# Performance work log

Hardware: AMD Instinct MI355X
Metric: run time of the kernel (lower is better)

## Reference

```python
import jax, jax.numpy as jnp
import numpy as np

B, L, D, H, W = 2, 4096, 1024, 16, 128
E = D // H

def _ln(x, g, b):
    m = jnp.mean(x, axis=-1, keepdims=True)
    v = jnp.mean((x - m) ** 2, axis=-1, keepdims=True)
    return (x - m) / jnp.sqrt(v + 1e-5) * g + b

def _swa(xn, Wqkv, bqkv, Wp, bp):
    # causal sliding-window attention: query i attends keys j in [i-W+1, i]
    b_, l_, d_ = xn.shape
    nb = l_ // W
    qkv = xn @ Wqkv + bqkv
    q, k, v = jnp.split(qkv, 3, axis=-1)
    def heads(t):
        return t.reshape(b_, l_, H, E).transpose(0, 2, 1, 3)  # [B,H,L,E]
    q, k, v = heads(q), heads(k), heads(v)
    def blk(t):
        return t.reshape(b_, H, nb, W, E)
    qb, kb, vb = blk(q), blk(k), blk(v)
    # each query block sees previous block + own block (covers the W-band)
    kprev = jnp.pad(kb, ((0, 0), (0, 0), (1, 0), (0, 0), (0, 0)))[:, :, :nb]
    vprev = jnp.pad(vb, ((0, 0), (0, 0), (1, 0), (0, 0), (0, 0)))[:, :, :nb]
    kc = jnp.concatenate([kprev, kb], axis=3)  # [B,H,nb,2W,E]
    vc = jnp.concatenate([vprev, vb], axis=3)
    scores = jnp.einsum('bhnre,bhnse->bhnrs', qb, kc) / np.float32(np.sqrt(E))
    r = jnp.arange(W)[:, None]
    s = jnp.arange(2 * W)[None, :]
    band = (s >= r + 1) & (s <= r + W)          # local coords of [i-W+1, i]
    first = band & (s >= W)                     # block 0 has no previous block
    mask = jnp.concatenate([first[None], jnp.broadcast_to(band, (nb - 1, W, 2 * W))], axis=0)
    scores = jnp.where(mask[None, None], scores, jnp.float32(-1e30))
    attn = jax.nn.softmax(scores, axis=-1)
    out = jnp.einsum('bhnrs,bhnse->bhnre', attn, vc)
    out = out.reshape(b_, H, l_, E).transpose(0, 2, 1, 3).reshape(b_, l_, d_)
    return out @ Wp + bp

def _linattn(xn, Wqkv, bqkv, Wo, bo):
    # chunked recurrent form of causal linear attention (same math as cumsum version)
    b_, l_, d_ = xn.shape
    C = 128
    nc = l_ // C
    qkv = xn @ Wqkv + bqkv
    q, k, v = jnp.split(qkv, 3, axis=-1)
    q = q.reshape(b_, l_, H, E)
    k = k.reshape(b_, l_, H, E)
    v = v.reshape(b_, l_, H, E)
    q = jax.nn.elu(q * np.float32(E ** -0.5)) + np.float32(1.0001)
    k = jax.nn.elu(k) + np.float32(1.0001)
    def chunks(t):
        return t.reshape(b_, nc, C, H, E).transpose(1, 0, 3, 2, 4)  # [nc,B,H,C,E]
    qc, kc, vc = chunks(q), chunks(k), chunks(v)
    tril = jnp.tril(jnp.ones((C, C), jnp.float32))
    def step(carry, inp):
        S, z = carry
        qi, ki, vi = inp
        A = jnp.einsum('bhce,bhde->bhcd', qi, ki) * tril
        num = jnp.einsum('bhce,bhef->bhcf', qi, S) + jnp.einsum('bhcd,bhdf->bhcf', A, vi)
        den = jnp.einsum('bhce,bhe->bhc', qi, z) + A.sum(-1)
        o = num / (den[..., None] + 1e-6)
        S = S + jnp.einsum('bhce,bhcf->bhef', ki, vi)
        z = z + ki.sum(2)
        return (S, z), o
    S0 = jnp.zeros((b_, H, E, E), jnp.float32)
    z0 = jnp.zeros((b_, H, E), jnp.float32)
    _, out = jax.lax.scan(step, (S0, z0), (qc, kc, vc))
    out = out.transpose(1, 0, 3, 2, 4).reshape(b_, l_, d_)
    return out @ Wo + bo

def setup_inputs() -> dict:
    key = jax.random.key(0)
    ks = jax.random.split(key, 9)
    def w(k, shape, s=0.02):
        return jax.random.normal(k, shape, jnp.float32) * s
    return {
        'x': jax.random.normal(ks[0], (B, L, D), jnp.float32),
        'g1': jnp.ones((D,), jnp.float32), 'b1': jnp.zeros((D,), jnp.float32),
        'Wqkv_a': w(ks[1], (D, 3 * D)), 'bqkv_a': jnp.zeros((3 * D,), jnp.float32),
        'Wp_a': w(ks[2], (D, D)), 'bp_a': jnp.zeros((D,), jnp.float32),
        'Wqkv_s': w(ks[3], (D, 3 * D)), 'bqkv_s': jnp.zeros((3 * D,), jnp.float32),
        'Wo_s': w(ks[4], (D, D)), 'bo_s': jnp.zeros((D,), jnp.float32),
        'Wo': w(ks[5], (D, D)), 'bo': jnp.zeros((D,), jnp.float32),
        'gm': jnp.ones((D,), jnp.float32), 'bm': jnp.zeros((D,), jnp.float32),
        'W1': w(ks[6], (D, 4 * D)), 'b1m': jnp.zeros((4 * D,), jnp.float32),
        'W2': w(ks[7], (4 * D, D)), 'b2m': jnp.zeros((D,), jnp.float32),
    }

def reference(x, g1, b1, Wqkv_a, bqkv_a, Wp_a, bp_a, Wqkv_s, bqkv_s, Wo_s, bo_s,
              Wo, bo, gm, bm, W1, b1m, W2, b2m):
    xn = _ln(x, g1, b1)
    attn_out = _swa(xn, Wqkv_a, bqkv_a, Wp_a, bp_a)
    ssm_out = _linattn(xn, Wqkv_s, bqkv_s, Wo_s, bo_s)
    mixed = (attn_out + ssm_out) @ Wo + bo
    x1 = x + mixed
    h = _ln(x1, gm, bm)
    mlp = jax.nn.gelu(h @ W1 + b1m, approximate=False) @ W2 + b2m
    return x1 + mlp
```

## Files before the change

### kernel.cpp

```cpp
#include <hip/hip_runtime.h>
#include <hip/hip_bf16.h>
#include <math.h>

typedef __hip_bfloat16 bf16;
typedef float f32x4 __attribute__((ext_vector_type(4)));
typedef short short8 __attribute__((ext_vector_type(8)));
typedef unsigned short u16x4 __attribute__((ext_vector_type(4)));
typedef unsigned short u16x8 __attribute__((ext_vector_type(8)));

#define AS1 __attribute__((address_space(1)))
#define AS3 __attribute__((address_space(3)))

__device__ __forceinline__ void gload16(const void* g, void* l) {
  __builtin_amdgcn_global_load_lds((const AS1 unsigned int*)g, (AS3 unsigned int*)l, 16, 0, 0);
}
__device__ __forceinline__ float b2f(unsigned short u) {
  union { unsigned int i; float f; } c; c.i = ((unsigned int)u) << 16; return c.f;
}
__device__ __forceinline__ unsigned short f2b(float f) {
  bf16 h = __float2bfloat16(f);
  unsigned short s; __builtin_memcpy(&s, &h, 2); return s;
}
__device__ __forceinline__ f32x4 mfma16(short8 a, short8 b, f32x4 c) {
  return __builtin_amdgcn_mfma_f32_16x16x32_bf16(a, b, c, 0, 0, 0);
}

#define BARR asm volatile("s_barrier" ::: "memory")
#define LGKM0 asm volatile("s_waitcnt lgkmcnt(0)" ::: "memory")
#define VM4 asm volatile("s_waitcnt vmcnt(4)" ::: "memory")
#define VM3 asm volatile("s_waitcnt vmcnt(3)" ::: "memory")
#define VM0 asm volatile("s_waitcnt vmcnt(0)" ::: "memory")
#define SB0 __builtin_amdgcn_sched_barrier(0)
#define PRIO1 __builtin_amdgcn_s_setprio(1)
#define PRIO0 __builtin_amdgcn_s_setprio(0)

__global__ __launch_bounds__(256) void ln_kernel(
    const float* __restrict__ X, const float* __restrict__ G,
    const float* __restrict__ Bb, unsigned short* __restrict__ Y) {
  __shared__ float red[8];
  const size_t row = blockIdx.x;
  const int tid = threadIdx.x;
  f32x4 v = *(const f32x4*)&X[row * 1024 + tid * 4];
  float s = 0.f, sq = 0.f;
#pragma unroll
  for (int j = 0; j < 4; ++j) { s += v[j]; sq += v[j] * v[j]; }
#pragma unroll
  for (int o = 1; o < 64; o <<= 1) { s += __shfl_xor(s, o); sq += __shfl_xor(sq, o); }
  if ((tid & 63) == 0) { red[tid >> 6] = s; red[4 + (tid >> 6)] = sq; }
  __syncthreads();
  s = red[0] + red[1] + red[2] + red[3];
  sq = red[4] + red[5] + red[6] + red[7];
  const float mean = s * (1.f / 1024.f);
  const float var = sq * (1.f / 1024.f) - mean * mean;
  const float inv = 1.f / sqrtf(var + 1e-5f);
  f32x4 gv = *(const f32x4*)&G[tid * 4];
  f32x4 bv = *(const f32x4*)&Bb[tid * 4];
  u16x4 ov;
#pragma unroll
  for (int j = 0; j < 4; ++j) ov[j] = f2b((v[j] - mean) * inv * gv[j] + bv[j]);
  *(u16x4*)&Y[row * 1024 + tid * 4] = ov;
}

__global__ __launch_bounds__(256) void transpose_w(
    const float* __restrict__ S, unsigned short* __restrict__ D,
    int N, int dld, int doff) {
  __shared__ __attribute__((aligned(16))) unsigned short t[64][72];
  const int k0 = blockIdx.x * 64, n0 = blockIdx.y * 64;
  const int tid = threadIdx.x;
#pragma unroll
  for (int i = 0; i < 2; ++i) {
    int c = i * 256 + tid;
    int row = c >> 3, c8 = c & 7;
    f32x4 a = *(const f32x4*)&S[(size_t)(k0 + row) * N + n0 + c8 * 8];
    f32x4 b = *(const f32x4*)&S[(size_t)(k0 + row) * N + n0 + c8 * 8 + 4];
    u16x8 o;
#pragma unroll
    for (int j = 0; j < 4; ++j) { o[j] = f2b(a[j]); o[4 + j] = f2b(b[j]); }
    *(u16x8*)&t[row][c8 * 8] = o;
  }
  __syncthreads();
#pragma unroll
  for (int i = 0; i < 2; ++i) {
    int c = i * 256 + tid;
    int nrow = c >> 3, k8 = c & 7;
    u16x8 o;
#pragma unroll
    for (int j = 0; j < 8; ++j) o[j] = t[k8 * 8 + j][nrow];
    *(u16x8*)&D[(size_t)(n0 + nrow) * dld + doff + k0 + k8 * 8] = o;
  }
}

__global__ __launch_bounds__(256) void bias_comb(
    const float* __restrict__ a, const float* __restrict__ b, float* __restrict__ o) {
  int i = blockIdx.x * 256 + threadIdx.x;
  o[i] = a[i] + b[i];
}

__global__ __launch_bounds__(256) void bias_cat(
    const float* __restrict__ a, const float* __restrict__ b, float* __restrict__ o, int N) {
  int i = blockIdx.x * 256 + threadIdx.x;
  o[i] = (i < N) ? a[i] : b[i - N];
}

#define EPI_STORE 0
#define EPI_GELU 1
#define EPI_RES 2

template <int EPI, int OF32>
__global__ __launch_bounds__(512, 2) void gemm_big(
    const unsigned short* __restrict__ A, const unsigned short* __restrict__ Bt,
    const float* __restrict__ bias, void* __restrict__ Cv,
    const float* __restrict__ res, int K, int ldA, int ldC) {
  __shared__ __attribute__((aligned(16))) unsigned short Abuf[2][2][16 * 512];
  __shared__ __attribute__((aligned(16))) unsigned short Bbuf[2][2][16 * 512];
  const int tid = threadIdx.x, lane = tid & 63, wv = tid >> 6;
  const int g = lane >> 4, r = lane & 15;
  const int wr = wv >> 2, wc = wv & 3;
  const size_t arow0 = (size_t)blockIdx.x * 256;
  const size_t brow0 = (size_t)blockIdx.y * 256;
  const size_t ldAs = (size_t)ldA, Ksz = (size_t)K;
  const unsigned short* gA0 = A + (arow0 + (size_t)((2 * wv + 0) * 16 + r)) * ldAs + g * 8;
  const unsigned short* gA1 = A + (arow0 + (size_t)((2 * wv + 1) * 16 + r)) * ldAs + g * 8;
  const unsigned short* gB0 = Bt + (brow0 + (size_t)((2 * wv + 0) * 16 + r)) * Ksz + g * 8;
  const unsigned short* gB1 = Bt + (brow0 + (size_t)((2 * wv + 1) * 16 + r)) * Ksz + g * 8;
  const int nT = K >> 6;
  f32x4 acc[8][4] = {};
  short8 af[8], bfr[4];

#define STG(BUF, KK, T_) do { size_t o_ = (size_t)(T_) * 64 + (KK) * 32;            \
    gload16(gA0 + o_, &Abuf[BUF][KK][(2 * wv + 0) * 512]);                           \
    gload16(gA1 + o_, &Abuf[BUF][KK][(2 * wv + 1) * 512]);                           \
    gload16(gB0 + o_, &Bbuf[BUF][KK][(2 * wv + 0) * 512]);                           \
    gload16(gB1 + o_, &Bbuf[BUF][KK][(2 * wv + 1) * 512]); } while (0)
#define PHASE(CUR, KK, T_)                                                           \
  do {                                                                               \
    const bool s1_ = (T_) + 1 < nT;                                                  \
    _Pragma("unroll") for (int m_ = 0; m_ < 8; ++m_)                                 \
      af[m_] = *(const short8*)&Abuf[CUR][KK][(wr * 8 + m_) * 512 + lane * 8];       \
    _Pragma("unroll") for (int n_ = 0; n_ < 4; ++n_)                                 \
      bfr[n_] = *(const short8*)&Bbuf[CUR][KK][(wc * 4 + n_) * 512 + lane * 8];      \
    if (s1_) STG(CUR ^ 1, KK, (T_) + 1);                                             \
    BARR; LGKM0; SB0;                                                                \
    PRIO1;                                                                           \
    _Pragma("unroll") for (int m_ = 0; m_ < 8; ++m_)                                 \
      _Pragma("unroll") for (int n_ = 0; n_ < 4; ++n_)                               \
        acc[m_][n_] = mfma16(af[m_], bfr[n_], acc[m_][n_]);                          \
    PRIO0;                                                                           \
    if (s1_) { VM4; } else if ((KK) == 0) { VM0; }                                   \
    BARR; SB0;                                                                       \
  } while (0)

  STG(0, 0, 0); STG(0, 1, 0);
  VM4; BARR; SB0;

  for (int T = 0; T < nT; ++T) {
    const int cur = T & 1;
    PHASE(cur, 0, T);
    PHASE(cur, 1, T);
  }
#undef PHASE
#undef STG

#pragma unroll
  for (int m = 0; m < 8; ++m) {
#pragma unroll
    for (int n = 0; n < 4; ++n) {
      const int col = (int)brow0 + wc * 64 + n * 16 + r;
      const float bv = bias[col];
#pragma unroll
      for (int i = 0; i < 4; ++i) {
        const size_t row = arow0 + wr * 128 + m * 16 + g * 4 + i;
        float v = acc[m][n][i] + bv;
        if (EPI == EPI_GELU) v = 0.5f * v * (1.f + erff(v * 0.70710678118f));
        if (EPI == EPI_RES) v += res[row * ldC + col];
        if (OF32) ((float*)Cv)[row * ldC + col] = v;
        else ((unsigned short*)Cv)[row * ldC + col] = f2b(v);
      }
    }
  }
}

template <int EPI, int OF32>
__global__ __launch_bounds__(512, 2) void gemm_sml(
    const unsigned short* __restrict__ A, const unsigned short* __restrict__ Bt,
    const float* __restrict__ bias, void* __restrict__ Cv,
    const float* __restrict__ res, int K, int ldA, int ldC) {
  __shared__ __attribute__((aligned(16))) unsigned short Abuf[2][2][8 * 512];
  __shared__ __attribute__((aligned(16))) unsigned short Bbuf[2][2][16 * 512];
  const int tid = threadIdx.x, lane = tid & 63, wv = tid >> 6;
  const int g = lane >> 4, r = lane & 15;
  const int wr = wv >> 2, wc = wv & 3;
  const size_t arow0 = (size_t)blockIdx.x * 128;
  const size_t brow0 = (size_t)blockIdx.y * 256;
  const size_t ldAs = (size_t)ldA, Ksz = (size_t)K;
  const unsigned short* gAs = A + (arow0 + (size_t)(wv * 16 + r)) * ldAs + g * 8;
  const unsigned short* gB0 = Bt + (brow0 + (size_t)((2 * wv + 0) * 16 + r)) * Ksz + g * 8;
  const unsigned short* gB1 = Bt + (brow0 + (size_t)((2 * wv + 1) * 16 + r)) * Ksz + g * 8;
  const int nT = K >> 6;
  f32x4 acc[4][4] = {};
  short8 af[4], bfr[4];

#define STG(BUF, KK, T_) do { size_t o_ = (size_t)(T_) * 64 + (KK) * 32;            \
    gload16(gAs + o_, &Abuf[BUF][KK][wv * 512]);                                     \
    gload16(gB0 + o_, &Bbuf[BUF][KK][(2 * wv + 0) * 512]);                           \
    gload16(gB1 + o_, &Bbuf[BUF][KK][(2 * wv + 1) * 512]); } while (0)
#define RD(CUR, KK) do {                                                             \
    _Pragma("unroll") for (int m_ = 0; m_ < 4; ++m_)                                 \
      af[m_] = *(const short8*)&Abuf[CUR][KK][(wr * 4 + m_) * 512 + lane * 8];       \
    _Pragma("unroll") for (int n_ = 0; n_ < 4; ++n_)                                 \
      bfr[n_] = *(const short8*)&Bbuf[CUR][KK][(wc * 4 + n_) * 512 + lane * 8]; } while (0)
#define MM() _Pragma("unroll") for (int m_ = 0; m_ < 4; ++m_)                        \
    _Pragma("unroll") for (int n_ = 0; n_ < 4; ++n_)                                 \
      acc[m_][n_] = mfma16(af[m_], bfr[n_], acc[m_][n_]);

  STG(0, 0, 0); STG(0, 1, 0);
  VM3; BARR; SB0;

  for (int T = 0; T < nT; ++T) {
    const int cur = T & 1;
    const bool s1 = (T + 1) < nT;
    RD(cur, 0);
    if (s1) STG(cur ^ 1, 0, T + 1);
    BARR; LGKM0; SB0;
    PRIO1; MM(); PRIO0;
    if (s1) { VM3; } else { VM0; }
    BARR; SB0;
    RD(cur, 1);
    if (s1) STG(cur ^ 1, 1, T + 1);
    BARR; LGKM0; SB0;
    PRIO1; MM(); PRIO0;
    if (s1) { VM3; }
    BARR; SB0;
  }
#undef STG
#undef RD
#undef MM

#pragma unroll
  for (int m = 0; m < 4; ++m) {
#pragma unroll
    for (int n = 0; n < 4; ++n) {
      const int col = (int)brow0 + wc * 64 + n * 16 + r;
      const float bv = bias[col];
#pragma unroll
      for (int i = 0; i < 4; ++i) {
        const size_t row = arow0 + wr * 64 + m * 16 + g * 4 + i;
        float v = acc[m][n][i] + bv;
        if (EPI == EPI_GELU) v = 0.5f * v * (1.f + erff(v * 0.70710678118f));
        if (EPI == EPI_RES) v += res[row * ldC + col];
        if (OF32) ((float*)Cv)[row * ldC + col] = v;
        else ((unsigned short*)Cv)[row * ldC + col] = f2b(v);
      }
    }
  }
}

__global__ __launch_bounds__(256) void swa_kernel(
    const unsigned short* __restrict__ qkv, unsigned short* __restrict__ outc) {
  __shared__ __attribute__((aligned(16))) unsigned short Ks[256 * 64];
  __shared__ __attribute__((aligned(16))) unsigned short Vt[64 * 264];
  __shared__ __attribute__((aligned(16))) unsigned short Ps[128 * 264];
  __shared__ __attribute__((aligned(16))) float dn[128];
  const int bid = blockIdx.x;
  const int qb = bid & 31, h = (bid >> 5) & 15, b = bid >> 9;
  const long btok = (long)b * 4096;
  const long tok0 = btok + (long)qb * 128;
  const int tid = threadIdx.x, lane = tid & 63, wv = tid >> 6;
  const int g = lane >> 4, r = lane & 15;

#pragma unroll
  for (int i = 0; i < 8; ++i) {
    int chunk = (wv * 8 + i) * 64 + lane;
    int s = chunk >> 3, cc = (chunk & 7) ^ (s & 7);
    long kt = tok0 - 128 + s; if (kt < btok) kt = btok;
    gload16(&qkv[(size_t)kt * 6144 + 1024 + h * 64 + cc * 8], &Ks[(wv * 8 + i) * 512]);
  }
#pragma unroll
  for (int i = 0; i < 8; ++i) {
    int chunk = i * 256 + tid;
    int s = chunk >> 3, e8 = chunk & 7;
    long kt = tok0 - 128 + s; if (kt < btok) kt = btok;
    u16x8 u = *(const u16x8*)&qkv[(size_t)kt * 6144 + 2048 + h * 64 + e8 * 8];
#pragma unroll
    for (int j = 0; j < 8; ++j) Vt[(e8 * 8 + j) * 264 + s] = u[j];
  }
  short8 qf[2][2];
#pragma unroll
  for (int m = 0; m < 2; ++m)
#pragma unroll
    for (int kc = 0; kc < 2; ++kc)
      qf[m][kc] = *(const short8*)&qkv[(size_t)(tok0 + wv * 32 + m * 16 + r) * 6144 + h * 64 + kc * 32 + g * 8];
  __syncthreads();

  float rs[2][4] = {};
  for (int n = 0; n < 16; ++n) {
    const int srow = n * 16 + r;
    short8 kf0 = *(const short8*)&Ks[srow * 64 + ((g) ^ (srow & 7)) * 8];
    short8 kf1 = *(const short8*)&Ks[srow * 64 + ((4 + g) ^ (srow & 7)) * 8];
#pragma unroll
    for (int m = 0; m < 2; ++m) {
      f32x4 acc = {0.f, 0.f, 0.f, 0.f};
      acc = mfma16(qf[m][0], kf0, acc);
      acc = mfma16(qf[m][1], kf1, acc);
#pragma unroll
      for (int i = 0; i < 4; ++i) {
        int rr = wv * 32 + m * 16 + g * 4 + i;
        int ss = n * 16 + r;
        bool valid = (ss >= rr + 1) && (ss <= rr + 128) && (qb > 0 || ss >= 128);
        float p = valid ? __expf(acc[i] * 0.125f) : 0.f;
        rs[m][i] += p;
        Ps[rr * 264 + ss] = f2b(p);
      }
    }
  }
#pragma unroll
  for (int m = 0; m < 2; ++m)
#pragma unroll
    for (int i = 0; i < 4; ++i) {
      float v = rs[m][i];
      v += __shfl_xor(v, 1); v += __shfl_xor(v, 2);
      v += __shfl_xor(v, 4); v += __shfl_xor(v, 8);
      if (r == i) dn[wv * 32 + m * 16 + g * 4 + i] = v;
    }
  __syncthreads();

  f32x4 oacc[2][4] = {};
  for (int sc = 0; sc < 8; ++sc) {
    short8 pf[2], vf[4];
#pragma unroll
    for (int m = 0; m < 2; ++m)
      pf[m] = *(const short8*)&Ps[(wv * 32 + m * 16 + r) * 264 + sc * 32 + g * 8];
#pragma unroll
    for (int n = 0; n < 4; ++n)
      vf[n] = *(const short8*)&Vt[(n * 16 + r) * 264 + sc * 32 + g * 8];
#pragma unroll
    for (int m = 0; m < 2; ++m)
#pragma unroll
      for (int n = 0; n < 4; ++n)
        oacc[m][n] = mfma16(pf[m], vf[n], oacc[m][n]);
  }
#pragma unroll
  for (int m = 0; m < 2; ++m) {
    f32x4 dv = *(const f32x4*)&dn[wv * 32 + m * 16 + g * 4];
#pragma unroll
    for (int n = 0; n < 4; ++n) {
      int col = h * 64 + n * 16 + r;
#pragma unroll
      for (int i = 0; i < 4; ++i) {
        size_t row = (size_t)(tok0 + wv * 32 + m * 16 + g * 4 + i);
        outc[row * 2048 + col] = f2b(oacc[m][n][i] / dv[i]);
      }
    }
  }
}

__global__ __launch_bounds__(256) void lin_pass1(
    const unsigned short* __restrict__ qkv, float* __restrict__ KVt, float* __restrict__ kz) {
  __shared__ __attribute__((aligned(16))) unsigned short kf[128 * 72];
  __shared__ __attribute__((aligned(16))) unsigned short vs[128 * 72];
  const int bid = blockIdx.x;
  const int ch = bid & 31, h = (bid >> 5) & 15, b = bid >> 9;
  const size_t tok0 = (size_t)b * 4096 + (size_t)ch * 128;
  const int tid = threadIdx.x;
#pragma unroll
  for (int i = 0; i < 4; ++i) {
    int c = i * 256 + tid;
    int row = c >> 3, e8 = c & 7;
    u16x8 uk = *(const u16x8*)&qkv[(tok0 + row) * 6144 + 1024 + h * 64 + e8 * 8];
    u16x8 uv = *(const u16x8*)&qkv[(tok0 + row) * 6144 + 2048 + h * 64 + e8 * 8];
    u16x8 tk;
#pragma unroll
    for (int j = 0; j < 8; ++j) {
      float x = b2f(uk[j]);
      x = (x > 0.f) ? x : expm1f(x);
      tk[j] = f2b(x + 1.0001f);
    }
    *(u16x8*)&kf[row * 72 + e8 * 8] = tk;
    *(u16x8*)&vs[row * 72 + e8 * 8] = uv;
  }
  __syncthreads();
  const int e0 = (tid & 15) * 4, f0 = (tid >> 4) * 4;
  float acc[4][4] = {};
  for (int c = 0; c < 128; ++c) {
    u16x4 ku = *(const u16x4*)&kf[c * 72 + e0];
    u16x4 vu = *(const u16x4*)&vs[c * 72 + f0];
    float ke[4], vv[4];
#pragma unroll
    for (int j = 0; j < 4; ++j) { ke[j] = b2f(ku[j]); vv[j] = b2f(vu[j]); }
#pragma unroll
    for (int jf = 0; jf < 4; ++jf)
#pragma unroll
      for (int je = 0; je < 4; ++je)
        acc[jf][je] += vv[jf] * ke[je];
  }
  const size_t base = (size_t)bid * 4096;
#pragma unroll
  for (int jf = 0; jf < 4; ++jf) {
    f32x4 o = {acc[jf][0], acc[jf][1], acc[jf][2], acc[jf][3]};
    *(f32x4*)&KVt[base + (f0 + jf) * 64 + e0] = o;
  }
  if (tid < 64) {
    float s = 0.f;
    for (int c = 0; c < 128; ++c) s += b2f(kf[c * 72 + tid]);
    kz[(size_t)bid * 64 + tid] = s;
  }
}

__global__ __launch_bounds__(256) void lin_pass2(float* __restrict__ KVt, float* __restrict__ kz) {
  const int bh = blockIdx.x;
  const int tid = threadIdx.x;
  f32x4 run[4] = {};
  for (int ch = 0; ch < 32; ++ch) {
    const size_t base = ((size_t)bh * 32 + ch) * 4096;
#pragma unroll
    for (int i = 0; i < 4; ++i) {
      float* p = &KVt[base + (size_t)(i * 256 + tid) * 4];
      f32x4 c = *(f32x4*)p;
      *(f32x4*)p = run[i];
      run[i] += c;
    }
  }
  if (tid < 64) {
    float rz = 0.f;
    for (int ch = 0; ch < 32; ++ch) {
      float* p = &kz[((size_t)bh * 32 + ch) * 64 + tid];
      float c = *p; *p = rz; rz += c;
    }
  }
}

__global__ __launch_bounds__(256) void lin_pass3(
    const unsigned short* __restrict__ qkv, const float* __restrict__ KVt,
    const float* __restrict__ kz, unsigned short* __restrict__ outc) {
  __shared__ __attribute__((aligned(16))) unsigned short qf[128 * 72];
  __shared__ __attribute__((aligned(16))) unsigned short kf[128 * 72];
  __shared__ __attribute__((aligned(16))) unsigned short vt[64 * 136];
  __shared__ __attribute__((aligned(16))) unsigned short st[64 * 72];
  __shared__ __attribute__((aligned(16))) unsigned short am[128 * 136];
  __shared__ __attribute__((aligned(16))) float zs[64];
  __shared__ __attribute__((aligned(16))) float dnl[128];
  const int bid = blockIdx.x;
  const int ch = bid & 31, h = (bid >> 5) & 15, b = bid >> 9;
  const size_t tok0 = (size_t)b * 4096 + (size_t)ch * 128;
  const int tid = threadIdx.x, lane = tid & 63, wv = tid >> 6;
  const int g = lane >> 4, r = lane & 15;

#pragma unroll
  for (int i = 0; i < 4; ++i) {
    int c = i * 256 + tid;
    int row = c >> 3, e8 = c & 7;
    u16x8 uq = *(const u16x8*)&qkv[(tok0 + row) * 6144 + h * 64 + e8 * 8];
    u16x8 uk = *(const u16x8*)&qkv[(tok0 + row) * 6144 + 1024 + h * 64 + e8 * 8];
    u16x8 uv = *(const u16x8*)&qkv[(tok0 + row) * 6144 + 2048 + h * 64 + e8 * 8];
    u16x8 tq, tk;
#pragma unroll
    for (int j = 0; j < 8; ++j) {
      float x = b2f(uq[j]) * 0.125f;
      x = (x > 0.f) ? x : expm1f(x);
      tq[j] = f2b(x + 1.0001f);
      float y = b2f(uk[j]);
      y = (y > 0.f) ? y : expm1f(y);
      tk[j] = f2b(y + 1.0001f);
    }
    *(u16x8*)&qf[row * 72 + e8 * 8] = tq;
    *(u16x8*)&kf[row * 72 + e8 * 8] = tk;
#pragma unroll
    for (int j = 0; j < 8; ++j) vt[(e8 * 8 + j) * 136 + row] = uv[j];
  }
#pragma unroll
  for (int i = 0; i < 2; ++i) {
    int idx = i * 256 + tid;
    int f = idx >> 3, e8 = idx & 7;
    f32x4 s0 = *(const f32x4*)&KVt[(size_t)bid * 4096 + f * 64 + e8 * 8];
    f32x4 s1 = *(const f32x4*)&KVt[(size_t)bid * 4096 + f * 64 + e8 * 8 + 4];
    u16x8 t;
#pragma unroll
    for (int j = 0; j < 4; ++j) { t[j] = f2b(s0[j]); t[4 + j] = f2b(s1[j]); }
    *(u16x8*)&st[f * 72 + e8 * 8] = t;
  }
  if (tid < 64) zs[tid] = kz[(size_t)bid * 64 + tid];
  __syncthreads();

  short8 aq[2][2];
#pragma unroll
  for (int m = 0; m < 2; ++m)
#pragma unroll
    for (int kc = 0; kc < 2; ++kc)
      aq[m][kc] = *(const short8*)&qf[(wv * 32 + m * 16 + r) * 72 + kc * 32 + g * 8];

  float rsA[2][4] = {};
  for (int n = 0; n < 8; ++n) {
    short8 bk0 = *(const short8*)&kf[(n * 16 + r) * 72 + g * 8];
    short8 bk1 = *(const short8*)&kf[(n * 16 + r) * 72 + 32 + g * 8];
#pragma unroll
    for (int m = 0; m < 2; ++m) {
      f32x4 acc = {0.f, 0.f, 0.f, 0.f};
      acc = mfma16(aq[m][0], bk0, acc);
      acc = mfma16(aq[m][1], bk1, acc);
#pragma unroll
      for (int i = 0; i < 4; ++i) {
        int rr = wv * 32 + m * 16 + g * 4 + i;
        int cc = n * 16 + r;
        float v = (cc <= rr) ? acc[i] : 0.f;
        rsA[m][i] += v;
        am[rr * 136 + cc] = f2b(v);
      }
    }
  }
#pragma unroll
  for (int m = 0; m < 2; ++m)
#pragma unroll
    for (int i = 0; i < 4; ++i) {
      float v = rsA[m][i];
      v += __shfl_xor(v, 1); v += __shfl_xor(v, 2);
      v += __shfl_xor(v, 4); v += __shfl_xor(v, 8);
      if (r == i) dnl[wv * 32 + m * 16 + g * 4 + i] = v;
    }
  __syncthreads();

  if (tid < 128) {
    float s = dnl[tid];
#pragma unroll
    for (int e = 0; e < 64; e += 4) {
      u16x4 qv = *(const u16x4*)&qf[tid * 72 + e];
      s += b2f(qv[0]) * zs[e] + b2f(qv[1]) * zs[e + 1] + b2f(qv[2]) * zs[e + 2] + b2f(qv[3]) * zs[e + 3];
    }
    dnl[tid] = s + 1e-6f;
  }

  f32x4 oac[2][4] = {};
#pragma unroll
  for (int kc = 0; kc < 2; ++kc) {
    short8 sf[4];
#pragma unroll
    for (int n = 0; n < 4; ++n) sf[n] = *(const short8*)&st[(n * 16 + r) * 72 + kc * 32 + g * 8];
#pragma unroll
    for (int m = 0; m < 2; ++m)
#pragma unroll
      for (int n = 0; n < 4; ++n)
        oac[m][n] = mfma16(aq[m][kc], sf[n], oac[m][n]);
  }
  for (int c4 = 0; c4 < 4; ++c4) {
    short8 pa[2], vb[4];
#pragma unroll
    for (int m = 0; m < 2; ++m)
      pa[m] = *(const short8*)&am[(wv * 32 + m * 16 + r) * 136 + c4 * 32 + g * 8];
#pragma unroll
    for (int n = 0; n < 4; ++n)
      vb[n] = *(const short8*)&vt[(n * 16 + r) * 136 + c4 * 32 + g * 8];
#pragma unroll
    for (int m = 0; m < 2; ++m)
#pragma unroll
      for (int n = 0; n < 4; ++n)
        oac[m][n] = mfma16(pa[m], vb[n], oac[m][n]);
  }
  __syncthreads();
#pragma unroll
  for (int m = 0; m < 2; ++m) {
    f32x4 dv = *(const f32x4*)&dnl[wv * 32 + m * 16 + g * 4];
#pragma unroll
    for (int n = 0; n < 4; ++n) {
      int col = 1024 + h * 64 + n * 16 + r;
#pragma unroll
      for (int i = 0; i < 4; ++i) {
        size_t row = tok0 + wv * 32 + m * 16 + g * 4 + i;
        outc[row * 2048 + col] = f2b(oac[m][n][i] / dv[i]);
      }
    }
  }
}

extern "C" void kernel_launch(void* const* d_in, const int* in_sizes, int n_in,
                              void* d_out, int out_size, void* d_ws, size_t ws_size,
                              hipStream_t stream) {
  (void)in_sizes; (void)n_in; (void)out_size; (void)ws_size;
  const float* x      = (const float*)d_in[0];
  const float* g1     = (const float*)d_in[1];
  const float* b1     = (const float*)d_in[2];
  const float* Wqkv_a = (const float*)d_in[3];
  const float* bqkv_a = (const float*)d_in[4];
  const float* Wp_a   = (const float*)d_in[5];
  const float* bp_a   = (const float*)d_in[6];
  const float* Wqkv_s = (const float*)d_in[7];
  const float* bqkv_s = (const float*)d_in[8];
  const float* Wo_s   = (const float*)d_in[9];
  const float* bo_s   = (const float*)d_in[10];
  const float* Wo     = (const float*)d_in[11];
  const float* bo     = (const float*)d_in[12];
  const float* gm     = (const float*)d_in[13];
  const float* bm     = (const float*)d_in[14];
  const float* W1     = (const float*)d_in[15];
  const float* b1m    = (const float*)d_in[16];
  const float* W2     = (const float*)d_in[17];
  const float* b2m    = (const float*)d_in[18];
  float* out = (float*)d_out;

  char* ws = (char*)d_ws;
  size_t off = 0;
  auto alloc = [&](size_t bytes) { char* p = ws + off; off += (bytes + 255) & ~(size_t)255; return p; };
  unsigned short* wTaS  = (unsigned short*)alloc((size_t)6144 * 1024 * 2);
  unsigned short* wTpo  = (unsigned short*)alloc((size_t)1024 * 2048 * 2);
  unsigned short* wTo   = (unsigned short*)alloc((size_t)1024 * 1024 * 2);
  unsigned short* wT1   = (unsigned short*)alloc((size_t)4096 * 1024 * 2);
  unsigned short* wT2   = (unsigned short*)alloc((size_t)1024 * 4096 * 2);
  float*          bcomb = (float*)alloc(1024 * 4);
  float*          bcat  = (float*)alloc(6144 * 4);
  unsigned short* xn    = (unsigned short*)alloc((size_t)8192 * 1024 * 2);
  unsigned short* qkvAS = (unsigned short*)alloc((size_t)8192 * 6144 * 2);
  unsigned short* comb  = (unsigned short*)alloc((size_t)8192 * 2048 * 2);
  float*          kvt   = (float*)alloc((size_t)1024 * 4096 * 4);
  float*          kzp   = (float*)alloc((size_t)1024 * 64 * 4);
  unsigned short* gbuf  = qkvAS;
  unsigned short* sum   = (unsigned short*)kvt;
  unsigned short* h_    = xn;
  float*          x1    = (float*)comb;

  transpose_w<<<dim3(16, 48), 256, 0, stream>>>(Wqkv_a, wTaS, 3072, 1024, 0);
  transpose_w<<<dim3(16, 48), 256, 0, stream>>>(Wqkv_s, wTaS + (size_t)3072 * 1024, 3072, 1024, 0);
  transpose_w<<<dim3(16, 16), 256, 0, stream>>>(Wp_a, wTpo, 1024, 2048, 0);
  transpose_w<<<dim3(16, 16), 256, 0, stream>>>(Wo_s, wTpo, 1024, 2048, 1024);
  transpose_w<<<dim3(16, 16), 256, 0, stream>>>(Wo, wTo, 1024, 1024, 0);
  transpose_w<<<dim3(16, 64), 256, 0, stream>>>(W1, wT1, 4096, 1024, 0);
  transpose_w<<<dim3(64, 16), 256, 0, stream>>>(W2, wT2, 1024, 4096, 0);
  bias_comb<<<4, 256, 0, stream>>>(bp_a, bo_s, bcomb);
  bias_cat<<<24, 256, 0, stream>>>(bqkv_a, bqkv_s, bcat, 3072);

  ln_kernel<<<8192, 256, 0, stream>>>(x, g1, b1, xn);
  gemm_big<EPI_STORE, 0><<<dim3(32, 24), 512, 0, stream>>>(xn, wTaS, bcat, qkvAS, nullptr, 1024, 1024, 6144);
  swa_kernel<<<1024, 256, 0, stream>>>(qkvAS, comb);
  lin_pass1<<<1024, 256, 0, stream>>>(qkvAS + 3072, kvt, kzp);
  lin_pass2<<<32, 256, 0, stream>>>(kvt, kzp);
  lin_pass3<<<1024, 256, 0, stream>>>(qkvAS + 3072, kvt, kzp, comb);
  gemm_sml<EPI_STORE, 0><<<dim3(64, 4), 512, 0, stream>>>(comb, wTpo, bcomb, sum, nullptr, 2048, 2048, 1024);
  gemm_sml<EPI_RES, 1><<<dim3(64, 4), 512, 0, stream>>>(sum, wTo, bo, x1, x, 1024, 1024, 1024);
  ln_kernel<<<8192, 256, 0, stream>>>(x1, gm, bm, h_);
  gemm_big<EPI_GELU, 0><<<dim3(32, 16), 512, 0, stream>>>(h_, wT1, b1m, gbuf, nullptr, 1024, 1024, 4096);
  gemm_sml<EPI_RES, 1><<<dim3(64, 4), 512, 0, stream>>>(gbuf, wT2, b2m, out, x1, 4096, 4096, 1024);
}
```

Measured before the change: 614.8 us.

## Swizzle GEMM block order per XCD and triple-buffer small GEMM pipeline

Both GEMM kernels now take a 1D grid and remap block IDs so that consecutive blocks scheduled round-robin across the 8 XCDs land on nearby tiles, improving L2 reuse of A/B panels. The small GEMM drops its 2x2 double buffer for a 3-stage ring of 32-wide K slices with prefetch distance two and one barrier pair per slice. Its launch bounds rise to 4 waves-per-SIMD occupancy hint. These changes aim to cut memory stalls and cache misses, at the risk of register pressure from the higher occupancy target and more barriers per K.

```diff
diff --git a/kernel.cpp b/kernel.cpp
--- a/kernel.cpp
+++ b/kernel.cpp
@@ -110,14 +110,17 @@
 __global__ __launch_bounds__(512, 2) void gemm_big(
     const unsigned short* __restrict__ A, const unsigned short* __restrict__ Bt,
     const float* __restrict__ bias, void* __restrict__ Cv,
-    const float* __restrict__ res, int K, int ldA, int ldC) {
+    const float* __restrict__ res, int K, int ldA, int ldC, int lgnmt) {
   __shared__ __attribute__((aligned(16))) unsigned short Abuf[2][2][16 * 512];
   __shared__ __attribute__((aligned(16))) unsigned short Bbuf[2][2][16 * 512];
   const int tid = threadIdx.x, lane = tid & 63, wv = tid >> 6;
   const int g = lane >> 4, r = lane & 15;
   const int wr = wv >> 2, wc = wv & 3;
-  const size_t arow0 = (size_t)blockIdx.x * 256;
-  const size_t brow0 = (size_t)blockIdx.y * 256;
+  const int bid = blockIdx.x, nwg = gridDim.x;
+  const int swz = (bid & 7) * (nwg >> 3) + (bid >> 3);
+  const int mt = swz & ((1 << lgnmt) - 1), nt = swz >> lgnmt;
+  const size_t arow0 = (size_t)mt * 256;
+  const size_t brow0 = (size_t)nt * 256;
   const size_t ldAs = (size_t)ldA, Ksz = (size_t)K;
   const unsigned short* gA0 = A + (arow0 + (size_t)((2 * wv + 0) * 16 + r)) * ldAs + g * 8;
   const unsigned short* gA1 = A + (arow0 + (size_t)((2 * wv + 1) * 16 + r)) * ldAs + g * 8;
@@ -181,60 +184,61 @@
 }
 
 template <int EPI, int OF32>
-__global__ __launch_bounds__(512, 2) void gemm_sml(
+__global__ __launch_bounds__(512, 4) void gemm_sml(
     const unsigned short* __restrict__ A, const unsigned short* __restrict__ Bt,
     const float* __restrict__ bias, void* __restrict__ Cv,
-    const float* __restrict__ res, int K, int ldA, int ldC) {
-  __shared__ __attribute__((aligned(16))) unsigned short Abuf[2][2][8 * 512];
-  __shared__ __attribute__((aligned(16))) unsigned short Bbuf[2][2][16 * 512];
+    const float* __restrict__ res, int K, int ldA, int ldC, int lgnmt) {
+  __shared__ __attribute__((aligned(16))) unsigned short Abuf[3][8 * 512];
+  __shared__ __attribute__((aligned(16))) unsigned short Bbuf[3][16 * 512];
   const int tid = threadIdx.x, lane = tid & 63, wv = tid >> 6;
   const int g = lane >> 4, r = lane & 15;
   const int wr = wv >> 2, wc = wv & 3;
-  const size_t arow0 = (size_t)blockIdx.x * 128;
-  const size_t brow0 = (size_t)blockIdx.y * 256;
+  const int bid = blockIdx.x, nwg = gridDim.x;
+  const int swz = (bid & 7) * (nwg >> 3) + (bid >> 3);
+  const int mt = swz & ((1 << lgnmt) - 1), nt = swz >> lgnmt;
+  const size_t arow0 = (size_t)mt * 128;
+  const size_t brow0 = (size_t)nt * 256;
   const size_t ldAs = (size_t)ldA, Ksz = (size_t)K;
   const unsigned short* gAs = A + (arow0 + (size_t)(wv * 16 + r)) * ldAs + g * 8;
   const unsigned short* gB0 = Bt + (brow0 + (size_t)((2 * wv + 0) * 16 + r)) * Ksz + g * 8;
   const unsigned short* gB1 = Bt + (brow0 + (size_t)((2 * wv + 1) * 16 + r)) * Ksz + g * 8;
-  const int nT = K >> 6;
+  const int nP = K >> 5;
   f32x4 acc[4][4] = {};
-  short8 af[4], bfr[4];
-
-#define STG(BUF, KK, T_) do { size_t o_ = (size_t)(T_) * 64 + (KK) * 32;            \
-    gload16(gAs + o_, &Abuf[BUF][KK][wv * 512]);                                     \
-    gload16(gB0 + o_, &Bbuf[BUF][KK][(2 * wv + 0) * 512]);                           \
-    gload16(gB1 + o_, &Bbuf[BUF][KK][(2 * wv + 1) * 512]); } while (0)
-#define RD(CUR, KK) do {                                                             \
-    _Pragma("unroll") for (int m_ = 0; m_ < 4; ++m_)                                 \
-      af[m_] = *(const short8*)&Abuf[CUR][KK][(wr * 4 + m_) * 512 + lane * 8];       \
-    _Pragma("unroll") for (int n_ = 0; n_ < 4; ++n_)                                 \
-      bfr[n_] = *(const short8*)&Bbuf[CUR][KK][(wc * 4 + n_) * 512 + lane * 8]; } while (0)
-#define MM() _Pragma("unroll") for (int m_ = 0; m_ < 4; ++m_)                        \
-    _Pragma("unroll") for (int n_ = 0; n_ < 4; ++n_)                                 \
-      acc[m_][n_] = mfma16(af[m_], bfr[n_], acc[m_][n_]);
-
-  STG(0, 0, 0); STG(0, 1, 0);
+
+#define STG(RG, P_) do { size_t o_ = (size_t)(P_) * 32;                              \
+    gload16(gAs + o_, &Abuf[RG][wv * 512]);                                          \
+    gload16(gB0 + o_, &Bbuf[RG][(2 * wv + 0) * 512]);                                \
+    gload16(gB1 + o_, &Bbuf[RG][(2 * wv + 1) * 512]); } while (0)
+
+  STG(0, 0); STG(1, 1);
   VM3; BARR; SB0;
 
-  for (int T = 0; T < nT; ++T) {
-    const int cur = T & 1;
-    const bool s1 = (T + 1) < nT;
-    RD(cur, 0);
-    if (s1) STG(cur ^ 1, 0, T + 1);
+  int rc = 0;
+  for (int p = 0; p < nP; ++p) {
+    const bool s2 = (p + 2) < nP;
+    const bool s1 = (p + 1) < nP;
+    int rs = rc + 2; if (rs >= 3) rs -= 3;
+    short8 af[4], bfr[4];
+#pragma unroll
+    for (int m = 0; m < 4; ++m)
+      af[m] = *(const short8*)&Abuf[rc][(wr * 4 + m) * 512 + lane * 8];
+#pragma unroll
+    for (int n = 0; n < 4; ++n)
+      bfr[n] = *(const short8*)&Bbuf[rc][(wc * 4 + n) * 512 + lane * 8];
+    if (s2) STG(rs, p + 2);
     BARR; LGKM0; SB0;
-    PRIO1; MM(); PRIO0;
-    if (s1) { VM3; } else { VM0; }
+    PRIO1;
+#pragma unroll
+    for (int m = 0; m < 4; ++m)
+#pragma unroll
+      for (int n = 0; n < 4; ++n)
+        acc[m][n] = mfma16(af[m], bfr[n], acc[m][n]);
+    PRIO0;
+    if (s2) { VM3; } else if (s1) { VM0; }
     BARR; SB0;
-    RD(cur, 1);
-    if (s1) STG(cur ^ 1, 1, T + 1);
-    BARR; LGKM0; SB0;
-    PRIO1; MM(); PRIO0;
-    if (s1) { VM3; }
-    BARR; SB0;
+    rc = (rc + 1 == 3) ? 0 : rc + 1;
   }
 #undef STG
-#undef RD
-#undef MM
 
 #pragma unroll
   for (int m = 0; m < 4; ++m) {
@@ -626,14 +630,14 @@
   bias_cat<<<24, 256, 0, stream>>>(bqkv_a, bqkv_s, bcat, 3072);
 
   ln_kernel<<<8192, 256, 0, stream>>>(x, g1, b1, xn);
-  gemm_big<EPI_STORE, 0><<<dim3(32, 24), 512, 0, stream>>>(xn, wTaS, bcat, qkvAS, nullptr, 1024, 1024, 6144);
+  gemm_big<EPI_STORE, 0><<<768, 512, 0, stream>>>(xn, wTaS, bcat, qkvAS, nullptr, 1024, 1024, 6144, 5);
   swa_kernel<<<1024, 256, 0, stream>>>(qkvAS, comb);
   lin_pass1<<<1024, 256, 0, stream>>>(qkvAS + 3072, kvt, kzp);
   lin_pass2<<<32, 256, 0, stream>>>(kvt, kzp);
   lin_pass3<<<1024, 256, 0, stream>>>(qkvAS + 3072, kvt, kzp, comb);
-  gemm_sml<EPI_STORE, 0><<<dim3(64, 4), 512, 0, stream>>>(comb, wTpo, bcomb, sum, nullptr, 2048, 2048, 1024);
-  gemm_sml<EPI_RES, 1><<<dim3(64, 4), 512, 0, stream>>>(sum, wTo, bo, x1, x, 1024, 1024, 1024);
+  gemm_sml<EPI_STORE, 0><<<256, 512, 0, stream>>>(comb, wTpo, bcomb, sum, nullptr, 2048, 2048, 1024, 6);
+  gemm_sml<EPI_RES, 1><<<256, 512, 0, stream>>>(sum, wTo, bo, x1, x, 1024, 1024, 1024, 6);
   ln_kernel<<<8192, 256, 0, stream>>>(x1, gm, bm, h_);
-  gemm_big<EPI_GELU, 0><<<dim3(32, 16), 512, 0, stream>>>(h_, wT1, b1m, gbuf, nullptr, 1024, 1024, 4096);
-  gemm_sml<EPI_RES, 1><<<dim3(64, 4), 512, 0, stream>>>(gbuf, wT2, b2m, out, x1, 4096, 4096, 1024);
-}
+  gemm_big<EPI_GELU, 0><<<512, 512, 0, stream>>>(h_, wT1, b1m, gbuf, nullptr, 1024, 1024, 4096, 5);
+  gemm_sml<EPI_RES, 1><<<256, 512, 0, stream>>>(gbuf, wT2, b2m, out, x1, 4096, 4096, 1024, 6);
+}
```

Result: slower. 628.5 us (+2.2%).
